# Optimization experiments

Hardware: AMD Instinct MI355X
Metric: run time of the kernel (lower is better)

The kernel has to match this reference:

```python
import jax, jax.numpy as jnp
import numpy as np

B, S, IN, OUT = 4, 32, 8192, 8192


def setup_inputs() -> dict:
    key = jax.random.key(0)
    k1, k2, k3, k4 = jax.random.split(key, 4)
    x = jax.random.normal(k1, (B, S, IN), dtype=jnp.float32)
    # FP8-e4m3 stored weight: round-trip through fp8 so values are representable,
    # then keep as fp32 (the module upcasts to fp32 before the matmul anyway).
    w = jax.random.normal(k2, (OUT, IN), dtype=jnp.float32)
    weight = w.astype(jnp.float8_e4m3fn).astype(jnp.float32)
    # per-output-channel scale, strictly positive small values
    weight_scale = jax.random.uniform(k3, (OUT, 1), dtype=jnp.float32,
                                      minval=1e-3, maxval=2e-2)
    bias = (jax.random.normal(k4, (OUT,), dtype=jnp.float32) * 0.01).astype(jnp.float16)
    return {"x": x, "weight": weight, "weight_scale": weight_scale, "bias": bias}


def reference(x, weight, weight_scale, bias):
    # dequantize fp8 weight to fp32 with per-channel scale  [OUT, IN]
    dq_w = weight * weight_scale
    # x @ dq_w.T  -> [B, S, OUT]
    out = jnp.einsum("bsi,oi->bso", x.astype(jnp.float32), dq_w)
    out = out + bias.astype(jnp.float32)
    return out
```

## Files before the change

kernel.cpp:

```cpp
#include <hip/hip_runtime.h>
#include <hip/hip_bf16.h>
#include <hip/hip_fp16.h>


namespace {
constexpr int NN = 8192;
constexpr int KK = 8192;
constexpr int KSPLIT = 4;
constexpr int KPB = KK / KSPLIT;
constexpr int BKT = 512;
constexpr int NIT = KPB / BKT;
constexpr size_t WS_NEED = (size_t)128 * KK * 2;

typedef __attribute__((ext_vector_type(8))) short bf16x8;
typedef __attribute__((ext_vector_type(4))) float f32x4;

__device__ __forceinline__ bf16x8 pack8(float4 a, float4 b) {
    union { __hip_bfloat16 h[8]; bf16x8 v; } p;
    p.h[0] = __float2bfloat16(a.x); p.h[1] = __float2bfloat16(a.y);
    p.h[2] = __float2bfloat16(a.z); p.h[3] = __float2bfloat16(a.w);
    p.h[4] = __float2bfloat16(b.x); p.h[5] = __float2bfloat16(b.y);
    p.h[6] = __float2bfloat16(b.z); p.h[7] = __float2bfloat16(b.w);
    return p.v;
}

__device__ __forceinline__ void gload_lds16(const void* g, void* l) {
    __builtin_amdgcn_global_load_lds(
        (const __attribute__((address_space(1))) unsigned int*)g,
        (__attribute__((address_space(3))) unsigned int*)l,
        16, 0, 0);
}
}

#define RAW_BARRIER() asm volatile("s_barrier" ::: "memory")
#define VMWAIT(N_)    asm volatile("s_waitcnt vmcnt(" #N_ ")" ::: "memory")

__global__ __launch_bounds__(256)
void cfp8_xprep(const float* __restrict__ x, unsigned char* __restrict__ ws)
{
    const int g = blockIdx.x * 256 + threadIdx.x;
    const float4* src = (const float4*)x + (size_t)g * 2;
    float4 a = src[0], b = src[1];
    const int m  = g >> 10;
    const int kg = g & 1023;
    const int s  = kg >> 2;
    const int r8 = kg & 3;
    const int t  = m >> 4;
    const int lm = m & 15;
    const int l  = r8 * 16 + lm;
    union { __hip_bfloat16 h[8]; uint4 u; } p;
    p.h[0] = __float2bfloat16(a.x); p.h[1] = __float2bfloat16(a.y);
    p.h[2] = __float2bfloat16(a.z); p.h[3] = __float2bfloat16(a.w);
    p.h[4] = __float2bfloat16(b.x); p.h[5] = __float2bfloat16(b.y);
    p.h[6] = __float2bfloat16(b.z); p.h[7] = __float2bfloat16(b.w);
    ((uint4*)ws)[(size_t)(s * 8 + t) * 64 + l] = p.u;
}

__global__ __launch_bounds__(256, 4)
void cfp8_gemm_r14(const float* __restrict__ w, const unsigned char* __restrict__ ws,
                   const float* __restrict__ c1, const float* __restrict__ c2,
                   float* __restrict__ out)
{
    __shared__ __align__(16) __hip_bfloat16 lw[32 * BKT];
    __shared__ int s_c1s, s_kind;

    const int tid  = threadIdx.x;
    const int lane = tid & 63;
    const int wid  = tid >> 6;
    const int l16  = lane & 15;
    const int quad = lane >> 4;
    const int bid  = blockIdx.x;
    const int kz   = bid & 3;
    const int n0   = (bid >> 2) * 32;
    const size_t kbase = (size_t)kz * KPB;

    if (tid < 64) {
        float v = c1[tid * 64];
        unsigned long long b = __ballot((v > 1e-4f) && (v < 0.5f));
        int c1s = (b == ~0ull) ? 1 : 0;
        const void* bp = c1s ? (const void*)c2 : (const void*)c1;
        float vf = __half2float(((const __half*)bp)[tid * 64]);
        unsigned long long bf_ = __ballot((vf < 0.5f) && (vf > -0.5f));
        float vb = __bfloat162float(((const __hip_bfloat16*)bp)[tid * 64]);
        unsigned long long bb = __ballot((vb < 0.5f) && (vb > -0.5f));
        if (tid == 0) {
            s_c1s  = c1s;
            s_kind = (bf_ == ~0ull) ? 0 : ((bb == ~0ull) ? 1 : 2);
        }
    }

    const int srow  = tid >> 3;
    const int scol8 = tid & 7;
    const float* wrow = w + (size_t)(n0 + srow) * KK + kbase + scol8 * 64;

    const uint4* xr = (const uint4*)ws;

    f32x4 acc[2][2];
#pragma unroll
    for (int i = 0; i < 2; ++i)
#pragma unroll
        for (int j = 0; j < 2; ++j) acc[i][j] = (f32x4){0.f, 0.f, 0.f, 0.f};

    for (int c = 0; c < NIT; ++c) {
        if (c) __syncthreads();

#pragma unroll 1
        for (int h = 0; h < 2; ++h) {
            float4 v[8];
#pragma unroll
            for (int i = 0; i < 8; ++i)
                v[i] = *(const float4*)(wrow + (size_t)c * BKT + h * 32 + i * 4);
#pragma unroll
            for (int p = 0; p < 4; ++p) {
                const int g = scol8 * 8 + h * 4 + p;
                bf16x8 ch = pack8(v[2 * p], v[2 * p + 1]);
                *(bf16x8*)((char*)lw + srow * 1024 + ((g ^ (srow & 7)) << 4)) = ch;
            }
        }
        __syncthreads();

        const int ksg0 = kz * 64 + c * 16;
#pragma unroll 4
        for (int ks = 0; ks < 16; ++ks) {
            bf16x8 af[2], bf[2];
#pragma unroll
            for (int i = 0; i < 2; ++i) {
                uint4 u = xr[(size_t)((ksg0 + ks) * 8 + wid * 2 + i) * 64 + lane];
                af[i] = *(bf16x8*)&u;
            }
#pragma unroll
            for (int j = 0; j < 2; ++j) {
                const int row_ = j * 16 + l16;
                const int kc   = ks * 4 + quad;
                bf[j] = *(const bf16x8*)((const char*)lw + row_ * 1024 +
                                         ((kc ^ (row_ & 7)) << 4));
            }
#pragma unroll
            for (int i = 0; i < 2; ++i)
#pragma unroll
                for (int j = 0; j < 2; ++j)
                    acc[i][j] = __builtin_amdgcn_mfma_f32_16x16x32_bf16(
                        af[i], bf[j], acc[i][j], 0, 0, 0);
        }
    }

    const float* scalep = s_c1s ? c1 : c2;
    const void*  biasp  = s_c1s ? (const void*)c2 : (const void*)c1;
#pragma unroll
    for (int j = 0; j < 2; ++j) {
        const int col = n0 + j * 16 + l16;
        const float scj = scalep[col];
        float bsj = 0.0f;
        if (kz == 0) {
            if (s_kind == 0)      bsj = __half2float(((const __half*)biasp)[col]);
            else if (s_kind == 1) bsj = __bfloat162float(((const __hip_bfloat16*)biasp)[col]);
            else                  bsj = ((const float*)biasp)[col];
        }
#pragma unroll
        for (int i = 0; i < 2; ++i) {
            const int mb = wid * 32 + i * 16 + quad * 4;
#pragma unroll
            for (int r = 0; r < 4; ++r)
                atomicAdd(out + (size_t)(mb + r) * NN + col,
                          acc[i][j][r] * scj + bsj);
        }
    }
}

__global__ __launch_bounds__(256, 1)
void cfp8_gemm_r12(const float* __restrict__ x, const float* __restrict__ w,
                   const float* __restrict__ c1, const float* __restrict__ c2,
                   float* __restrict__ out)
{
    constexpr int BKF = 32;
    constexpr int NITF = KPB / BKF;
    __shared__ __align__(16) float ldsA[4][128 * BKF];
    __shared__ __align__(16) float ldsB[4][128 * BKF];
    __shared__ int s_c1s, s_kind;

    const int tid  = threadIdx.x;
    const int lane = tid & 63;
    const int wid  = tid >> 6;
    const int l16  = lane & 15;
    const int quad = lane >> 4;
    const int wr   = wid >> 1;
    const int wc   = wid & 1;
    const int bid  = blockIdx.x;
    const int kz   = bid & 3;
    const int nb0  = (bid >> 2) * 128;
    const size_t kbase = (size_t)kz * KPB;

    if (tid < 64) {
        float v = c1[tid * 64];
        unsigned long long b = __ballot((v > 1e-4f) && (v < 0.5f));
        int c1s = (b == ~0ull) ? 1 : 0;
        const void* bp = c1s ? (const void*)c2 : (const void*)c1;
        float vf = __half2float(((const __half*)bp)[tid * 64]);
        unsigned long long bf_ = __ballot((vf < 0.5f) && (vf > -0.5f));
        float vb = __bfloat162float(((const __hip_bfloat16*)bp)[tid * 64]);
        unsigned long long bb = __ballot((vb < 0.5f) && (vb > -0.5f));
        if (tid == 0) {
            s_c1s  = c1s;
            s_kind = (bf_ == ~0ull) ? 0 : ((bb == ~0ull) ? 1 : 2);
        }
    }
    __syncthreads();

    unsigned off[4];
#pragma unroll
    for (int j = 0; j < 4; ++j) {
        const int q   = (wid * 4 + j) * 64 + lane;
        const int row = q >> 3;
        const int c8  = q & 7;
        const int swz = c8 ^ (row & 7);
        off[j] = (unsigned)row * (KK * 4) + (unsigned)swz * 16;
    }
    const char* xsrc = (const char*)(x + kbase);
    const char* wsrc = (const char*)(w + (size_t)nb0 * KK + kbase);

#define STAGE(slot_, c_)                                                       \
    {                                                                          \
        const size_t kb_ = (size_t)(c_) * (BKF * 4);                           \
        _Pragma("unroll")                                                      \
        for (int j = 0; j < 4; ++j) {                                          \
            gload_lds16(xsrc + kb_ + off[j],                                   \
                        (char*)&ldsA[slot_][0] + (wid * 4 + j) * 1024);        \
            gload_lds16(wsrc + kb_ + off[j],                                   \
                        (char*)&ldsB[slot_][0] + (wid * 4 + j) * 1024);        \
        }                                                                      \
    }
#define LOADFRAG(dst_, base_, rb_)                                             \
    {                                                                          \
        const int row_ = (rb_) + l16;                                          \
        const int sw_  = row_ & 7;                                             \
        float4 a0_ = *(const float4*)&(base_)[(row_ * 8 + ((quad * 2) ^ sw_)) * 4];     \
        float4 a1_ = *(const float4*)&(base_)[(row_ * 8 + ((quad * 2 + 1) ^ sw_)) * 4]; \
        dst_ = pack8(a0_, a1_);                                                \
    }
#define COMPUTE(slot_)                                                         \
    {                                                                          \
        const float* la_ = &ldsA[slot_][0];                                    \
        const float* lb_ = &ldsB[slot_][0];                                    \
        bf16x8 af_[4], bf_[4];                                                 \
        _Pragma("unroll")                                                      \
        for (int i = 0; i < 4; ++i) LOADFRAG(af_[i], la_, wr * 64 + i * 16)    \
        _Pragma("unroll")                                                      \
        for (int j = 0; j < 4; ++j) LOADFRAG(bf_[j], lb_, wc * 64 + j * 16)    \
        _Pragma("unroll")                                                      \
        for (int i = 0; i < 4; ++i)                                            \
            _Pragma("unroll")                                                  \
            for (int j = 0; j < 4; ++j)                                        \
                acc[i][j] = __builtin_amdgcn_mfma_f32_16x16x32_bf16(           \
                    af_[i], bf_[j], acc[i][j], 0, 0, 0);                       \
    }

    f32x4 acc[4][4];
#pragma unroll
    for (int i = 0; i < 4; ++i)
#pragma unroll
        for (int j = 0; j < 4; ++j) acc[i][j] = (f32x4){0.f, 0.f, 0.f, 0.f};

    STAGE(0, 0)
    STAGE(1, 1)
    STAGE(2, 2)
    for (int c = 0; c < NITF - 3; ++c) {
        VMWAIT(16);
        RAW_BARRIER();
        STAGE((c + 3) & 3, c + 3)
        COMPUTE(c & 3)
    }
    VMWAIT(16); RAW_BARRIER(); COMPUTE((NITF - 3) & 3)
    VMWAIT(8);  RAW_BARRIER(); COMPUTE((NITF - 2) & 3)
    VMWAIT(0);  RAW_BARRIER(); COMPUTE((NITF - 1) & 3)
#undef STAGE
#undef LOADFRAG
#undef COMPUTE

    const float* scalep = s_c1s ? c1 : c2;
    const void*  biasp  = s_c1s ? (const void*)c2 : (const void*)c1;
#pragma unroll
    for (int j = 0; j < 4; ++j) {
        const int col = nb0 + wc * 64 + j * 16 + l16;
        const float scj = scalep[col];
        float bsj = 0.0f;
        if (kz == 0) {
            if (s_kind == 0)      bsj = __half2float(((const __half*)biasp)[col]);
            else if (s_kind == 1) bsj = __bfloat162float(((const __hip_bfloat16*)biasp)[col]);
            else                  bsj = ((const float*)biasp)[col];
        }
#pragma unroll
        for (int i = 0; i < 4; ++i) {
            const int rb = wr * 64 + i * 16 + quad * 4;
#pragma unroll
            for (int r = 0; r < 4; ++r)
                atomicAdd(out + (size_t)(rb + r) * NN + col,
                          acc[i][j][r] * scj + bsj);
        }
    }
}

extern "C" void kernel_launch(void* const* d_in, const int* in_sizes, int n_in,
                              void* d_out, int out_size, void* d_ws, size_t ws_size,
                              hipStream_t stream) {
    int iw = 0;
    for (int i = 1; i < n_in; ++i) if (in_sizes[i] > in_sizes[iw]) iw = i;
    int ix = -1;
    for (int i = 0; i < n_in; ++i)
        if (i != iw && (ix < 0 || in_sizes[i] > in_sizes[ix])) ix = i;
    const float* c1 = nullptr;
    const float* c2 = nullptr;
    for (int i = 0; i < n_in; ++i) {
        if (i == iw || i == ix) continue;
        if (!c1) c1 = (const float*)d_in[i];
        else     c2 = (const float*)d_in[i];
    }
    const float* w = (const float*)d_in[iw];
    const float* x = (const float*)d_in[ix];
    float* out = (float*)d_out;

    hipMemsetAsync(d_out, 0, (size_t)out_size * sizeof(float), stream);

    if (d_ws != nullptr && ws_size >= WS_NEED) {
        unsigned char* ws = (unsigned char*)d_ws;
        cfp8_xprep<<<dim3(512), dim3(256), 0, stream>>>(x, ws);
        cfp8_gemm_r14<<<dim3(256 * KSPLIT), dim3(256), 0, stream>>>(w, ws, c1, c2, out);
    } else {
        cfp8_gemm_r12<<<dim3(64 * KSPLIT), dim3(256), 0, stream>>>(x, w, c1, c2, out);
    }
}
```

Measured before the change: 380.5 us.

## Replace atomic split-K accumulation with partial buffers and a reduce kernel

The GEMM kernel now writes each K-split's partial tile to its own workspace buffer instead of doing atomicAdd into the output. A new reduce kernel sums the four partials and applies the per-channel scale and bias, which also removes the output memset. The fp32 weight loads are reorganised so each wave reads whole rows with lane-contiguous float4 accesses, giving coalesced global loads before the bf16 conversion into LDS. This costs about 16 MB of extra partial-buffer traffic, an extra launch, and a much larger workspace requirement; if the workspace is too small the code falls back to the older r12 kernel.

```diff
diff --git a/kernel.cpp b/kernel.cpp
--- a/kernel.cpp
+++ b/kernel.cpp
@@ -10,7 +10,11 @@
 constexpr int KPB = KK / KSPLIT;
 constexpr int BKT = 512;
 constexpr int NIT = KPB / BKT;
-constexpr size_t WS_NEED = (size_t)128 * KK * 2;
+
+constexpr size_t XOFF = 0;
+constexpr size_t POFF = (size_t)128 * KK * 2;
+constexpr size_t PSZ  = (size_t)128 * NN * 4;
+constexpr size_t WS_NEED = POFF + (size_t)KSPLIT * PSZ;
 
 typedef __attribute__((ext_vector_type(8))) short bf16x8;
 typedef __attribute__((ext_vector_type(4))) float f32x4;
@@ -53,16 +57,14 @@
     p.h[2] = __float2bfloat16(a.z); p.h[3] = __float2bfloat16(a.w);
     p.h[4] = __float2bfloat16(b.x); p.h[5] = __float2bfloat16(b.y);
     p.h[6] = __float2bfloat16(b.z); p.h[7] = __float2bfloat16(b.w);
-    ((uint4*)ws)[(size_t)(s * 8 + t) * 64 + l] = p.u;
+    ((uint4*)(ws + XOFF))[(size_t)(s * 8 + t) * 64 + l] = p.u;
 }
 
 __global__ __launch_bounds__(256, 4)
-void cfp8_gemm_r14(const float* __restrict__ w, const unsigned char* __restrict__ ws,
-                   const float* __restrict__ c1, const float* __restrict__ c2,
-                   float* __restrict__ out)
+void cfp8_gemm_r15(const float* __restrict__ w, const unsigned char* __restrict__ ws,
+                   float* __restrict__ part)
 {
     __shared__ __align__(16) __hip_bfloat16 lw[32 * BKT];
-    __shared__ int s_c1s, s_kind;
 
     const int tid  = threadIdx.x;
     const int lane = tid & 63;
@@ -74,6 +76,91 @@
     const int n0   = (bid >> 2) * 32;
     const size_t kbase = (size_t)kz * KPB;
 
+    const uint4* xr = (const uint4*)(ws + XOFF);
+
+    f32x4 acc[2][2];
+#pragma unroll
+    for (int i = 0; i < 2; ++i)
+#pragma unroll
+        for (int j = 0; j < 2; ++j) acc[i][j] = (f32x4){0.f, 0.f, 0.f, 0.f};
+
+    for (int c = 0; c < NIT; ++c) {
+        if (c) __syncthreads();
+
+#pragma unroll 1
+        for (int rg = 0; rg < 2; ++rg) {
+            float4 v[4][2];
+#pragma unroll
+            for (int rr = 0; rr < 4; ++rr) {
+                const int r = wid * 8 + rg * 4 + rr;
+                const float* src = w + (size_t)(n0 + r) * KK + kbase + c * BKT;
+                v[rr][0] = *(const float4*)(src + lane * 4);
+                v[rr][1] = *(const float4*)(src + 256 + lane * 4);
+            }
+#pragma unroll
+            for (int rr = 0; rr < 4; ++rr) {
+                const int r = wid * 8 + rg * 4 + rr;
+#pragma unroll
+                for (int i = 0; i < 2; ++i) {
+                    const int g = i * 32 + (lane >> 1);
+                    union { __hip_bfloat16 h[4]; uint2 u; } p;
+                    p.h[0] = __float2bfloat16(v[rr][i].x);
+                    p.h[1] = __float2bfloat16(v[rr][i].y);
+                    p.h[2] = __float2bfloat16(v[rr][i].z);
+                    p.h[3] = __float2bfloat16(v[rr][i].w);
+                    *(uint2*)((char*)lw + r * 1024 +
+                              ((g ^ (r & 7)) << 4) + (lane & 1) * 8) = p.u;
+                }
+            }
+        }
+        __syncthreads();
+
+        const int ksg0 = kz * 64 + c * 16;
+#pragma unroll 4
+        for (int ks = 0; ks < 16; ++ks) {
+            bf16x8 af[2], bf[2];
+#pragma unroll
+            for (int i = 0; i < 2; ++i) {
+                uint4 u = xr[(size_t)((ksg0 + ks) * 8 + wid * 2 + i) * 64 + lane];
+                af[i] = *(bf16x8*)&u;
+            }
+#pragma unroll
+            for (int j = 0; j < 2; ++j) {
+                const int row_ = j * 16 + l16;
+                const int kc   = ks * 4 + quad;
+                bf[j] = *(const bf16x8*)((const char*)lw + row_ * 1024 +
+                                         ((kc ^ (row_ & 7)) << 4));
+            }
+#pragma unroll
+            for (int i = 0; i < 2; ++i)
+#pragma unroll
+                for (int j = 0; j < 2; ++j)
+                    acc[i][j] = __builtin_amdgcn_mfma_f32_16x16x32_bf16(
+                        af[i], bf[j], acc[i][j], 0, 0, 0);
+        }
+    }
+
+    float* pk = part + (size_t)kz * (PSZ / 4);
+#pragma unroll
+    for (int j = 0; j < 2; ++j) {
+        const int col = n0 + j * 16 + l16;
+#pragma unroll
+        for (int i = 0; i < 2; ++i) {
+            const int mb = wid * 32 + i * 16 + quad * 4;
+#pragma unroll
+            for (int r = 0; r < 4; ++r)
+                pk[(size_t)(mb + r) * NN + col] = acc[i][j][r];
+        }
+    }
+}
+
+__global__ __launch_bounds__(256)
+void cfp8_reduce(const float* __restrict__ part,
+                 const float* __restrict__ c1, const float* __restrict__ c2,
+                 float* __restrict__ out)
+{
+    __shared__ int s_c1s, s_kind;
+    const int tid = threadIdx.x;
     if (tid < 64) {
         float v = c1[tid * 64];
         unsigned long long b = __ballot((v > 1e-4f) && (v < 0.5f));
@@ -88,83 +175,34 @@
             s_kind = (bf_ == ~0ull) ? 0 : ((bb == ~0ull) ? 1 : 2);
         }
     }
-
-    const int srow  = tid >> 3;
-    const int scol8 = tid & 7;
-    const float* wrow = w + (size_t)(n0 + srow) * KK + kbase + scol8 * 64;
-
-    const uint4* xr = (const uint4*)ws;
-
-    f32x4 acc[2][2];
-#pragma unroll
-    for (int i = 0; i < 2; ++i)
-#pragma unroll
-        for (int j = 0; j < 2; ++j) acc[i][j] = (f32x4){0.f, 0.f, 0.f, 0.f};
-
-    for (int c = 0; c < NIT; ++c) {
-        if (c) __syncthreads();
-
-#pragma unroll 1
-        for (int h = 0; h < 2; ++h) {
-            float4 v[8];
-#pragma unroll
-            for (int i = 0; i < 8; ++i)
-                v[i] = *(const float4*)(wrow + (size_t)c * BKT + h * 32 + i * 4);
-#pragma unroll
-            for (int p = 0; p < 4; ++p) {
-                const int g = scol8 * 8 + h * 4 + p;
-                bf16x8 ch = pack8(v[2 * p], v[2 * p + 1]);
-                *(bf16x8*)((char*)lw + srow * 1024 + ((g ^ (srow & 7)) << 4)) = ch;
-            }
-        }
-        __syncthreads();
-
-        const int ksg0 = kz * 64 + c * 16;
-#pragma unroll 4
-        for (int ks = 0; ks < 16; ++ks) {
-            bf16x8 af[2], bf[2];
-#pragma unroll
-            for (int i = 0; i < 2; ++i) {
-                uint4 u = xr[(size_t)((ksg0 + ks) * 8 + wid * 2 + i) * 64 + lane];
-                af[i] = *(bf16x8*)&u;
-            }
-#pragma unroll
-            for (int j = 0; j < 2; ++j) {
-                const int row_ = j * 16 + l16;
-                const int kc   = ks * 4 + quad;
-                bf[j] = *(const bf16x8*)((const char*)lw + row_ * 1024 +
-                                         ((kc ^ (row_ & 7)) << 4));
-            }
-#pragma unroll
-            for (int i = 0; i < 2; ++i)
-#pragma unroll
-                for (int j = 0; j < 2; ++j)
-                    acc[i][j] = __builtin_amdgcn_mfma_f32_16x16x32_bf16(
-                        af[i], bf[j], acc[i][j], 0, 0, 0);
-        }
-    }
-
+    __syncthreads();
+
+    const int g = blockIdx.x * 256 + tid;
+    const float4* p4 = (const float4*)part;
+    float4 s = p4[g];
+#pragma unroll
+    for (int kz = 1; kz < KSPLIT; ++kz) {
+        float4 p = p4[(size_t)kz * (PSZ / 16) + g];
+        s.x += p.x; s.y += p.y; s.z += p.z; s.w += p.w;
+    }
+
+    const int n = (g & 2047) * 4;
     const float* scalep = s_c1s ? c1 : c2;
     const void*  biasp  = s_c1s ? (const void*)c2 : (const void*)c1;
-#pragma unroll
-    for (int j = 0; j < 2; ++j) {
-        const int col = n0 + j * 16 + l16;
-        const float scj = scalep[col];
-        float bsj = 0.0f;
-        if (kz == 0) {
-            if (s_kind == 0)      bsj = __half2float(((const __half*)biasp)[col]);
-            else if (s_kind == 1) bsj = __bfloat162float(((const __hip_bfloat16*)biasp)[col]);
-            else                  bsj = ((const float*)biasp)[col];
-        }
-#pragma unroll
-        for (int i = 0; i < 2; ++i) {
-            const int mb = wid * 32 + i * 16 + quad * 4;
-#pragma unroll
-            for (int r = 0; r < 4; ++r)
-                atomicAdd(out + (size_t)(mb + r) * NN + col,
-                          acc[i][j][r] * scj + bsj);
-        }
-    }
+    float4 sc = *(const float4*)(scalep + n);
+    float bs[4];
+#pragma unroll
+    for (int r = 0; r < 4; ++r) {
+        if (s_kind == 0)      bs[r] = __half2float(((const __half*)biasp)[n + r]);
+        else if (s_kind == 1) bs[r] = __bfloat162float(((const __hip_bfloat16*)biasp)[n + r]);
+        else                  bs[r] = ((const float*)biasp)[n + r];
+    }
+    float4 o;
+    o.x = s.x * sc.x + bs[0];
+    o.y = s.y * sc.y + bs[1];
+    o.z = s.z * sc.z + bs[2];
+    o.w = s.w * sc.w + bs[3];
+    ((float4*)out)[g] = o;
 }
 
 __global__ __launch_bounds__(256, 1)
@@ -200,7 +238,7 @@
         float vb = __bfloat162float(((const __hip_bfloat16*)bp)[tid * 64]);
         unsigned long long bb = __ballot((vb < 0.5f) && (vb > -0.5f));
         if (tid == 0) {
-            s_c1s  = c1s;
+            s_c1s = c1s;
             s_kind = (bf_ == ~0ull) ? 0 : ((bb == ~0ull) ? 1 : 2);
         }
     }
@@ -318,13 +356,14 @@
     const float* x = (const float*)d_in[ix];
     float* out = (float*)d_out;
 
-    hipMemsetAsync(d_out, 0, (size_t)out_size * sizeof(float), stream);
-
     if (d_ws != nullptr && ws_size >= WS_NEED) {
         unsigned char* ws = (unsigned char*)d_ws;
+        float* part = (float*)(ws + POFF);
         cfp8_xprep<<<dim3(512), dim3(256), 0, stream>>>(x, ws);
-        cfp8_gemm_r14<<<dim3(256 * KSPLIT), dim3(256), 0, stream>>>(w, ws, c1, c2, out);
+        cfp8_gemm_r15<<<dim3(256 * KSPLIT), dim3(256), 0, stream>>>(w, ws, part);
+        cfp8_reduce<<<dim3(1024), dim3(256), 0, stream>>>(part, c1, c2, out);
     } else {
+        hipMemsetAsync(d_out, 0, (size_t)out_size * sizeof(float), stream);
         cfp8_gemm_r12<<<dim3(64 * KSPLIT), dim3(256), 0, stream>>>(x, w, c1, c2, out);
     }
 }
```

Result: no change. 383.8 us (+0.9%).
